# Kernel tuning notes

Measured on AMD Instinct MI355X. Metric: run time of the kernel, lower is better.

## Reference

```python
import jax, jax.numpy as jnp
import numpy as np

PS = 32    # base patch size
SUB = 16   # subdivided patch size produced by sigmoid_round for up-weighted patches


def _sigmoid_round_np(x):
    # mirrors torch: round(32*sigmoid(x-24) + 16*(1-sigmoid(x-24)))
    s = 1.0 / (1.0 + np.exp(-(x - 24.0)))
    return np.round(32.0 * s + 16.0 * (1.0 - s)).astype(np.int64)


def _build_importance(P):
    # deterministic importance weights: even patches slightly above the mean
    # (-> adaptive size 16, subdivided), odd patches below (-> size 32, kept).
    avg = 1.0 / P
    a = avg * (2.0 ** (1.0 / 12.0)) * 1.001
    b = 2.0 * avg - a
    iw = np.empty(P, np.float64)
    iw[0::2] = a
    iw[1::2] = b
    return iw


def _build_token_index(P, G):
    # Reproduces the torch module's per-patch structural decision at trace time
    # (numpy on deterministic constants -> static shapes, jit-safe).
    iw = _build_importance(P)
    avg = iw.mean()
    sizes = _sigmoid_round_np(PS * (avg ** 12) / (iw ** 12))
    tok = []
    for i in range(P):
        r, c = i // G, i % G
        if 7 < sizes[i] < PS:  # subdivided into (PS/SUB)^2 = 4 sub-patches, row-major
            for dr in range(PS // SUB):
                for dc in range(PS // SUB):
                    tok.append(G * G + (2 * r + dr) * (2 * G) + (2 * c + dc))
        else:                   # full 32x32 patch token
            tok.append(r * G + c)
    return np.asarray(tok, np.int32)


def setup_inputs() -> dict:
    key = jax.random.key(0)
    k1, k2, k3 = jax.random.split(key, 3)
    B, C, H, E = 32, 3, 512, 768
    x = jax.random.normal(k1, (B, C, H, H), jnp.float32)
    patch_weight = jax.random.normal(k2, (E, C, PS, PS), jnp.float32) * 0.02
    patch_bias = jax.random.normal(k3, (E,), jnp.float32) * 0.02
    P = (H // PS) ** 2
    importance_w = jnp.asarray(_build_importance(P), jnp.float32)
    return {"x": x, "importance_w": importance_w, "patch_weight": patch_weight,
            "patch_bias": patch_bias, "num_patches": P}


def reference(x, importance_w, patch_weight, patch_bias, num_patches):
    B, C, H, _ = x.shape
    E = patch_weight.shape[0]
    G = H // PS            # 32x32 patch grid side
    kd = PS // SUB         # kernel divisor = 2
    tok_idx = _build_token_index(num_patches, G)  # static gather structure

    # full-size patches: stride-PS conv on each 32x32 tile == one GEMM
    # x tiles: (b, c, r, i, q, j) with row = r*PS+i, col = q*PS+j
    full = jnp.einsum('bcriqj,ecij->brqe',
                      x.reshape(B, C, G, PS, G, PS), patch_weight) + patch_bias

    # averaged 16x16 kernel: view(E,C,kd,kd,SUB,SUB).mean(dim=2).mean(dim=2)
    w_sub = patch_weight.reshape(E, C, kd, kd, SUB, SUB).mean(axis=(2, 3))
    sub = jnp.einsum('bcriqj,ecij->brqe',
                     x.reshape(B, C, kd * G, SUB, kd * G, SUB), w_sub) + patch_bias

    # token pool: [full 32-tiles (G*G), then all 16-tiles ((2G)^2)]; gather in
    # original patch order with subdivided patches expanded in place.
    pool = jnp.concatenate([full.reshape(B, G * G, E),
                            sub.reshape(B, (kd * G) ** 2, E)], axis=1)
    return pool[:, tok_idx, :]
```

## Files before the change

kernel.cpp:

```cpp
#include <hip/hip_runtime.h>
#include <stdint.h>


typedef __attribute__((ext_vector_type(8))) short bf16x8;
typedef __attribute__((ext_vector_type(4))) float f32x4;

__device__ __forceinline__ unsigned short f2bf(float f) {
  union { float f; unsigned u; } v; v.f = f;
  return (unsigned short)((v.u + 0x7fffu + ((v.u >> 16) & 1u)) >> 16);
}

__global__ __launch_bounds__(256) void prep_wfull(const float* __restrict__ pw,
                                                  unsigned short* __restrict__ Wf) {
  int g = blockIdx.x * 256 + threadIdx.x;
  float4 v = ((const float4*)pw)[g];
  ((ushort4*)Wf)[g] = make_ushort4(f2bf(v.x), f2bf(v.y), f2bf(v.z), f2bf(v.w));
}

__global__ __launch_bounds__(256) void prep_wsub(const float* __restrict__ pw,
                                                 unsigned short* __restrict__ Ws) {
  int g = blockIdx.x * 256 + threadIdx.x;
  int e = g / 192;
  int rem = g - e * 192;
  int cc = rem >> 6, r2 = rem & 63, s = r2 >> 2, t4 = r2 & 3;
  const float* base = pw + ((size_t)((e * 3 + cc) * 32 + (s >> 1)) * 32
                            + 16 * (s & 1) + 4 * t4);
  float4 q0 = *(const float4*)(base);
  float4 q1 = *(const float4*)(base + 8 * 32);
  float4 q2 = *(const float4*)(base + 16 * 32);
  float4 q3 = *(const float4*)(base + 24 * 32);
  ((ushort4*)Ws)[g] = make_ushort4(
      f2bf(0.25f * (q0.x + q1.x + q2.x + q3.x)),
      f2bf(0.25f * (q0.y + q1.y + q2.y + q3.y)),
      f2bf(0.25f * (q0.z + q1.z + q2.z + q3.z)),
      f2bf(0.25f * (q0.w + q1.w + q2.w + q3.w)));
}

__global__ __launch_bounds__(256) void gather_full(const float* __restrict__ x,
                                                   unsigned short* __restrict__ Af) {
  int g = blockIdx.x * 256 + threadIdx.x;
  int m = g / 768;
  int q = g - m * 768;
  int b = m >> 7, p = m & 127;
  int i = 2 * p + 1;
  int r = i >> 4, cpat = i & 15;
  int cc = q >> 8, rem = q & 255, ii = rem >> 3, jj4 = rem & 7;
  const float4* src = (const float4*)(x + ((size_t)((b * 3 + cc) * 512 + (r * 32 + ii)) * 512
                                           + cpat * 32 + jj4 * 4));
  float4 v = *src;
  ((ushort4*)Af)[g] = make_ushort4(f2bf(v.x), f2bf(v.y), f2bf(v.z), f2bf(v.w));
}

__global__ __launch_bounds__(256) void gather_sub(const float* __restrict__ x,
                                                  unsigned short* __restrict__ Asub) {
  int g = blockIdx.x * 256 + threadIdx.x;
  int m = g / 192;
  int q = g - m * 192;
  int b = m >> 9, t = m & 511;
  int p = t >> 2, s = t & 3, dr = s >> 1, dc = s & 1;
  int i = 2 * p;
  int r = i >> 4, cpat = i & 15;
  int cc = q >> 6, rem = q & 63, ii = rem >> 2, jj4 = rem & 3;
  int srow = r * 32 + dr * 16 + ii;
  int scol = cpat * 32 + dc * 16 + jj4 * 4;
  const float4* src = (const float4*)(x + ((size_t)((b * 3 + cc) * 512 + srow) * 512 + scol));
  float4 v = *src;
  ((ushort4*)Asub)[g] = make_ushort4(f2bf(v.x), f2bf(v.y), f2bf(v.z), f2bf(v.w));
}

__global__ __launch_bounds__(256) void gemm_kernel(
    const unsigned short* __restrict__ Af, const unsigned short* __restrict__ Asub,
    const unsigned short* __restrict__ Wf, const unsigned short* __restrict__ Ws,
    const float* __restrict__ bias, float* __restrict__ out) {
  __shared__ unsigned short Asm[128 * 64];
  __shared__ unsigned short Bsm[128 * 64];

  int bid = blockIdx.x;
  const unsigned short* Aptr;
  const unsigned short* Bptr;
  int K, bm, bn, which;
  if (bid < 192) {
    which = 0; bm = bid / 6; bn = bid - (bid / 6) * 6;
    Aptr = Af + (size_t)bm * 128 * 3072; Bptr = Wf; K = 3072;
  } else {
    int id = bid - 192;
    which = 1; bm = id / 6; bn = id - (id / 6) * 6;
    Aptr = Asub + (size_t)bm * 128 * 768; Bptr = Ws; K = 768;
  }
  const unsigned short* Brow = Bptr + (size_t)bn * 128 * K;

  int t = threadIdx.x;
  int lane = t & 63;
  int wv = t >> 6, wr = wv >> 1, wc = wv & 1;
  int lr = lane & 15, lk = lane >> 4;

  f32x4 acc[4][4];
#pragma unroll
  for (int mm = 0; mm < 4; ++mm)
#pragma unroll
    for (int nn = 0; nn < 4; ++nn) acc[mm][nn] = (f32x4){0.f, 0.f, 0.f, 0.f};

  const unsigned short* a_src = Aptr + (size_t)(t >> 3) * K + (t & 7) * 8;
  const unsigned short* b_src = Brow + (size_t)(t >> 3) * K + (t & 7) * 8;
  unsigned short* as_dst = &Asm[t * 8];
  unsigned short* bs_dst = &Bsm[t * 8];

  for (int k0 = 0; k0 < K; k0 += 64) {
#pragma unroll
    for (int is = 0; is < 4; ++is) {
      __builtin_amdgcn_global_load_lds(
          (const __attribute__((address_space(1))) void*)(a_src + (size_t)is * 32 * K + k0),
          (__attribute__((address_space(3))) void*)(as_dst + is * 2048), 16, 0, 0);
      __builtin_amdgcn_global_load_lds(
          (const __attribute__((address_space(1))) void*)(b_src + (size_t)is * 32 * K + k0),
          (__attribute__((address_space(3))) void*)(bs_dst + is * 2048), 16, 0, 0);
    }
    __syncthreads();
#pragma unroll
    for (int kk = 0; kk < 64; kk += 32) {
      bf16x8 af[4], bf[4];
#pragma unroll
      for (int mm = 0; mm < 4; ++mm)
        af[mm] = *(const bf16x8*)&Asm[(wr * 64 + mm * 16 + lr) * 64 + kk + lk * 8];
#pragma unroll
      for (int nn = 0; nn < 4; ++nn)
        bf[nn] = *(const bf16x8*)&Bsm[(wc * 64 + nn * 16 + lr) * 64 + kk + lk * 8];
#pragma unroll
      for (int mm = 0; mm < 4; ++mm)
#pragma unroll
        for (int nn = 0; nn < 4; ++nn)
          acc[mm][nn] = __builtin_amdgcn_mfma_f32_16x16x32_bf16(af[mm], bf[nn], acc[mm][nn], 0, 0, 0);
    }
    __syncthreads();
  }

#pragma unroll
  for (int mm = 0; mm < 4; ++mm) {
    int trow = wr * 64 + mm * 16 + lk * 4;
#pragma unroll
    for (int reg = 0; reg < 4; ++reg) {
      int grow = bm * 128 + trow + reg;
      size_t obase;
      if (which == 0) {
        int b = grow >> 7, p = grow & 127;
        obase = (size_t)(b * 640 + 5 * p + 4) * 768;
      } else {
        int b = grow >> 9, tt = grow & 511, p = tt >> 2, s = tt & 3;
        obase = (size_t)(b * 640 + 5 * p + s) * 768;
      }
#pragma unroll
      for (int nn = 0; nn < 4; ++nn) {
        int gcol = bn * 128 + wc * 64 + nn * 16 + lr;
        out[obase + gcol] = acc[mm][nn][reg] + bias[gcol];
      }
    }
  }
}

extern "C" void kernel_launch(void* const* d_in, const int* in_sizes, int n_in,
                              void* d_out, int out_size, void* d_ws, size_t ws_size,
                              hipStream_t stream) {
  const float* x  = (const float*)d_in[0];
  const float* pw = (const float*)d_in[2];
  const float* pb = (const float*)d_in[3];
  float* out = (float*)d_out;

  unsigned short* Af   = (unsigned short*)d_ws;
  unsigned short* Asub = Af + 12582912;
  unsigned short* Wf   = Asub + 12582912;
  unsigned short* Ws   = Wf + 2359296;

  prep_wfull<<<2304, 256, 0, stream>>>(pw, Wf);
  prep_wsub<<<576, 256, 0, stream>>>(pw, Ws);
  gather_full<<<12288, 256, 0, stream>>>(x, Af);
  gather_sub<<<12288, 256, 0, stream>>>(x, Asub);
  gemm_kernel<<<960, 256, 0, stream>>>(Af, Asub, Wf, Ws, pb, out);
}
```

Measured before the change: 258.6 us.

## Split-K the full-patch GEMM, fuse prep kernels, and interleave block scheduling

```diff
diff --git a/kernel.cpp b/kernel.cpp
--- a/kernel.cpp
+++ b/kernel.cpp
@@ -9,85 +9,91 @@
   union { float f; unsigned u; } v; v.f = f;
   return (unsigned short)((v.u + 0x7fffu + ((v.u >> 16) & 1u)) >> 16);
 }
-
-__global__ __launch_bounds__(256) void prep_wfull(const float* __restrict__ pw,
-                                                  unsigned short* __restrict__ Wf) {
-  int g = blockIdx.x * 256 + threadIdx.x;
-  float4 v = ((const float4*)pw)[g];
-  ((ushort4*)Wf)[g] = make_ushort4(f2bf(v.x), f2bf(v.y), f2bf(v.z), f2bf(v.w));
-}
-
-__global__ __launch_bounds__(256) void prep_wsub(const float* __restrict__ pw,
-                                                 unsigned short* __restrict__ Ws) {
-  int g = blockIdx.x * 256 + threadIdx.x;
-  int e = g / 192;
-  int rem = g - e * 192;
-  int cc = rem >> 6, r2 = rem & 63, s = r2 >> 2, t4 = r2 & 3;
-  const float* base = pw + ((size_t)((e * 3 + cc) * 32 + (s >> 1)) * 32
-                            + 16 * (s & 1) + 4 * t4);
-  float4 q0 = *(const float4*)(base);
-  float4 q1 = *(const float4*)(base + 8 * 32);
-  float4 q2 = *(const float4*)(base + 16 * 32);
-  float4 q3 = *(const float4*)(base + 24 * 32);
-  ((ushort4*)Ws)[g] = make_ushort4(
-      f2bf(0.25f * (q0.x + q1.x + q2.x + q3.x)),
-      f2bf(0.25f * (q0.y + q1.y + q2.y + q3.y)),
-      f2bf(0.25f * (q0.z + q1.z + q2.z + q3.z)),
-      f2bf(0.25f * (q0.w + q1.w + q2.w + q3.w)));
-}
-
-__global__ __launch_bounds__(256) void gather_full(const float* __restrict__ x,
-                                                   unsigned short* __restrict__ Af) {
-  int g = blockIdx.x * 256 + threadIdx.x;
-  int m = g / 768;
-  int q = g - m * 768;
-  int b = m >> 7, p = m & 127;
-  int i = 2 * p + 1;
-  int r = i >> 4, cpat = i & 15;
-  int cc = q >> 8, rem = q & 255, ii = rem >> 3, jj4 = rem & 7;
-  const float4* src = (const float4*)(x + ((size_t)((b * 3 + cc) * 512 + (r * 32 + ii)) * 512
-                                           + cpat * 32 + jj4 * 4));
-  float4 v = *src;
-  ((ushort4*)Af)[g] = make_ushort4(f2bf(v.x), f2bf(v.y), f2bf(v.z), f2bf(v.w));
-}
-
-__global__ __launch_bounds__(256) void gather_sub(const float* __restrict__ x,
-                                                  unsigned short* __restrict__ Asub) {
-  int g = blockIdx.x * 256 + threadIdx.x;
-  int m = g / 192;
-  int q = g - m * 192;
-  int b = m >> 9, t = m & 511;
-  int p = t >> 2, s = t & 3, dr = s >> 1, dc = s & 1;
-  int i = 2 * p;
-  int r = i >> 4, cpat = i & 15;
-  int cc = q >> 6, rem = q & 63, ii = rem >> 2, jj4 = rem & 3;
-  int srow = r * 32 + dr * 16 + ii;
-  int scol = cpat * 32 + dc * 16 + jj4 * 4;
-  const float4* src = (const float4*)(x + ((size_t)((b * 3 + cc) * 512 + srow) * 512 + scol));
-  float4 v = *src;
-  ((ushort4*)Asub)[g] = make_ushort4(f2bf(v.x), f2bf(v.y), f2bf(v.z), f2bf(v.w));
+__device__ __forceinline__ float bf2f(unsigned short h) {
+  union { unsigned u; float f; } v; v.u = ((unsigned)h) << 16; return v.f;
+}
+
+__global__ __launch_bounds__(256) void prep_gather(
+    const float* __restrict__ x, const float* __restrict__ pw,
+    unsigned short* __restrict__ Wf, unsigned short* __restrict__ Ws,
+    unsigned short* __restrict__ Af, unsigned short* __restrict__ Asub) {
+  int bid = blockIdx.x, t = threadIdx.x;
+  if (bid < 2304) {
+    int g = bid * 256 + t;
+    float4 v = ((const float4*)pw)[g];
+    ((ushort4*)Wf)[g] = make_ushort4(f2bf(v.x), f2bf(v.y), f2bf(v.z), f2bf(v.w));
+  } else if (bid < 2880) {
+    int g = (bid - 2304) * 256 + t;
+    int e = g / 192;
+    int rem = g - e * 192;
+    int cc = rem >> 6, r2 = rem & 63, s = r2 >> 2, t4 = r2 & 3;
+    const float* base = pw + ((size_t)((e * 3 + cc) * 32 + (s >> 1)) * 32
+                              + 16 * (s & 1) + 4 * t4);
+    float4 q0 = *(const float4*)(base);
+    float4 q1 = *(const float4*)(base + 8 * 32);
+    float4 q2 = *(const float4*)(base + 16 * 32);
+    float4 q3 = *(const float4*)(base + 24 * 32);
+    ((ushort4*)Ws)[g] = make_ushort4(
+        f2bf(0.25f * (q0.x + q1.x + q2.x + q3.x)),
+        f2bf(0.25f * (q0.y + q1.y + q2.y + q3.y)),
+        f2bf(0.25f * (q0.z + q1.z + q2.z + q3.z)),
+        f2bf(0.25f * (q0.w + q1.w + q2.w + q3.w)));
+  } else if (bid < 15168) {
+    int g = (bid - 2880) * 256 + t;
+    int m = g / 768, q = g - m * 768;
+    int b = m >> 7, p = m & 127;
+    int i = 2 * p + 1;
+    int r = i >> 4, cpat = i & 15;
+    int cc = q >> 8, rem = q & 255, ii = rem >> 3, jj4 = rem & 7;
+    const float4* src = (const float4*)(x + ((size_t)((b * 3 + cc) * 512 + (r * 32 + ii)) * 512
+                                             + cpat * 32 + jj4 * 4));
+    float4 v = *src;
+    ((ushort4*)Af)[g] = make_ushort4(f2bf(v.x), f2bf(v.y), f2bf(v.z), f2bf(v.w));
+  } else {
+    int g = (bid - 15168) * 256 + t;
+    int m = g / 192, q = g - m * 192;
+    int b = m >> 9, tt = m & 511;
+    int p = tt >> 2, s = tt & 3, dr = s >> 1, dc = s & 1;
+    int i = 2 * p;
+    int r = i >> 4, cpat = i & 15;
+    int cc = q >> 6, rem = q & 63, ii = rem >> 2, jj4 = rem & 3;
+    int srow = r * 32 + dr * 16 + ii;
+    int scol = cpat * 32 + dc * 16 + jj4 * 4;
+    const float4* src = (const float4*)(x + ((size_t)((b * 3 + cc) * 512 + srow) * 512 + scol));
+    float4 v = *src;
+    ((ushort4*)Asub)[g] = make_ushort4(f2bf(v.x), f2bf(v.y), f2bf(v.z), f2bf(v.w));
+  }
 }
 
 __global__ __launch_bounds__(256) void gemm_kernel(
     const unsigned short* __restrict__ Af, const unsigned short* __restrict__ Asub,
     const unsigned short* __restrict__ Wf, const unsigned short* __restrict__ Ws,
-    const float* __restrict__ bias, float* __restrict__ out) {
+    const float* __restrict__ bias, unsigned short* __restrict__ Pf,
+    float* __restrict__ out) {
   __shared__ unsigned short Asm[128 * 64];
   __shared__ unsigned short Bsm[128 * 64];
 
-  int bid = blockIdx.x;
-  const unsigned short* Aptr;
-  const unsigned short* Bptr;
-  int K, bm, bn, which;
-  if (bid < 192) {
-    which = 0; bm = bid / 6; bn = bid - (bid / 6) * 6;
-    Aptr = Af + (size_t)bm * 128 * 3072; Bptr = Wf; K = 3072;
+  int bid = (blockIdx.x & 7) * 192 + (blockIdx.x >> 3);
+
+  const unsigned short* Abase;
+  const unsigned short* Bbase;
+  int rsA, bm, bn, kofs, which, kc = 0;
+  if (bid < 768) {
+    which = 0;
+    int grp = bid / 6; bn = bid - grp * 6;
+    bm = grp >> 2; kc = grp & 3;
+    rsA = 3072; kofs = kc * 768;
+    Abase = Af + (size_t)bm * 128 * 3072;
+    Bbase = Wf;
   } else {
-    int id = bid - 192;
-    which = 1; bm = id / 6; bn = id - (id / 6) * 6;
-    Aptr = Asub + (size_t)bm * 128 * 768; Bptr = Ws; K = 768;
-  }
-  const unsigned short* Brow = Bptr + (size_t)bn * 128 * K;
+    which = 1;
+    int id = bid - 768;
+    bm = id / 6; bn = id - bm * 6;
+    rsA = 768; kofs = 0;
+    Abase = Asub + (size_t)bm * 128 * 768;
+    Bbase = Ws;
+  }
+  const unsigned short* Brow = Bbase + (size_t)bn * 128 * rsA;
 
   int t = threadIdx.x;
   int lane = t & 63;
@@ -100,19 +106,19 @@
 #pragma unroll
     for (int nn = 0; nn < 4; ++nn) acc[mm][nn] = (f32x4){0.f, 0.f, 0.f, 0.f};
 
-  const unsigned short* a_src = Aptr + (size_t)(t >> 3) * K + (t & 7) * 8;
-  const unsigned short* b_src = Brow + (size_t)(t >> 3) * K + (t & 7) * 8;
+  const unsigned short* a_src = Abase + (size_t)(t >> 3) * rsA + (t & 7) * 8 + kofs;
+  const unsigned short* b_src = Brow + (size_t)(t >> 3) * rsA + (t & 7) * 8 + kofs;
   unsigned short* as_dst = &Asm[t * 8];
   unsigned short* bs_dst = &Bsm[t * 8];
 
-  for (int k0 = 0; k0 < K; k0 += 64) {
+  for (int k0 = 0; k0 < 768; k0 += 64) {
 #pragma unroll
     for (int is = 0; is < 4; ++is) {
       __builtin_amdgcn_global_load_lds(
-          (const __attribute__((address_space(1))) void*)(a_src + (size_t)is * 32 * K + k0),
+          (const __attribute__((address_space(1))) void*)(a_src + (size_t)is * 32 * rsA + k0),
           (__attribute__((address_space(3))) void*)(as_dst + is * 2048), 16, 0, 0);
       __builtin_amdgcn_global_load_lds(
-          (const __attribute__((address_space(1))) void*)(b_src + (size_t)is * 32 * K + k0),
+          (const __attribute__((address_space(1))) void*)(b_src + (size_t)is * 32 * rsA + k0),
           (__attribute__((address_space(3))) void*)(bs_dst + is * 2048), 16, 0, 0);
     }
     __syncthreads();
@@ -140,21 +146,41 @@
 #pragma unroll
     for (int reg = 0; reg < 4; ++reg) {
       int grow = bm * 128 + trow + reg;
-      size_t obase;
       if (which == 0) {
-        int b = grow >> 7, p = grow & 127;
-        obase = (size_t)(b * 640 + 5 * p + 4) * 768;
+        unsigned short* pdst = Pf + ((size_t)(kc * 4096 + grow)) * 768;
+#pragma unroll
+        for (int nn = 0; nn < 4; ++nn) {
+          int gcol = bn * 128 + wc * 64 + nn * 16 + lr;
+          pdst[gcol] = f2bf(acc[mm][nn][reg]);
+        }
       } else {
-        int b = grow >> 9, tt = grow & 511, p = tt >> 2, s = tt & 3;
-        obase = (size_t)(b * 640 + 5 * p + s) * 768;
-      }
-#pragma unroll
-      for (int nn = 0; nn < 4; ++nn) {
-        int gcol = bn * 128 + wc * 64 + nn * 16 + lr;
-        out[obase + gcol] = acc[mm][nn][reg] + bias[gcol];
+        int b = grow >> 9, tt2 = grow & 511, p = tt2 >> 2, s = tt2 & 3;
+        size_t obase = (size_t)(b * 640 + 5 * p + s) * 768;
+#pragma unroll
+        for (int nn = 0; nn < 4; ++nn) {
+          int gcol = bn * 128 + wc * 64 + nn * 16 + lr;
+          out[obase + gcol] = acc[mm][nn][reg] + bias[gcol];
+        }
       }
     }
   }
+}
+
+__global__ __launch_bounds__(256) void reduce_full(
+    const unsigned short* __restrict__ Pf, const float* __restrict__ bias,
+    float* __restrict__ out) {
+  int q = blockIdx.x * 256 + threadIdx.x;
+  int m = q / 192, c4 = q - m * 192;
+  float4 sacc = ((const float4*)bias)[c4];
+#pragma unroll
+  for (int kc = 0; kc < 4; ++kc) {
+    ushort4 u = ((const ushort4*)(Pf + ((size_t)(kc * 4096 + m)) * 768))[c4];
+    sacc.x += bf2f(u.x); sacc.y += bf2f(u.y);
+    sacc.z += bf2f(u.z); sacc.w += bf2f(u.w);
+  }
+  int b = m >> 7, p = m & 127;
+  size_t obase = (size_t)(b * 640 + 5 * p + 4) * 768;
+  ((float4*)(out + obase))[c4] = sacc;
 }
 
 extern "C" void kernel_launch(void* const* d_in, const int* in_sizes, int n_in,
@@ -169,10 +195,9 @@
   unsigned short* Asub = Af + 12582912;
   unsigned short* Wf   = Asub + 12582912;
   unsigned short* Ws   = Wf + 2359296;
-
-  prep_wfull<<<2304, 256, 0, stream>>>(pw, Wf);
-  prep_wsub<<<576, 256, 0, stream>>>(pw, Ws);
-  gather_full<<<12288, 256, 0, stream>>>(x, Af);
-  gather_sub<<<12288, 256, 0, stream>>>(x, Asub);
-  gemm_kernel<<<960, 256, 0, stream>>>(Af, Asub, Wf, Ws, pb, out);
-}
+  unsigned short* Pf   = Ws + 589824;
+
+  prep_gather<<<27456, 256, 0, stream>>>(x, pw, Wf, Ws, Af, Asub);
+  gemm_kernel<<<1536, 256, 0, stream>>>(Af, Asub, Wf, Ws, pb, Pf, out);
+  reduce_full<<<3072, 256, 0, stream>>>(Pf, pb, out);
+}
```

After: 255.2 us. About the same (-1.3%).
